# Kernel tuning notes

Hardware: AMD Instinct MI355X
Metric: run time of the kernel (lower is better)

Reference implementation:

```python
import jax, jax.numpy as jnp
import numpy as np

B, S, D, H = 2, 2048, 1024, 16
HD = D // H  # head_dim = 64
NEG = -1.0e9


def setup_inputs() -> dict:
    key = jax.random.key(0)
    ks = jax.random.split(key, 6)
    scale = 1.0 / np.sqrt(D)
    x = jax.random.normal(ks[0], (B, S, D), dtype=jnp.float32)
    # causal additive mask: 1.0 where position is masked (future), matching scores += mask * -1e9
    mask = jnp.triu(jnp.ones((S, S), dtype=jnp.float32), k=1)[None, None, :, :]
    wq = jax.random.normal(ks[1], (D, D), dtype=jnp.float32) * scale
    wk = jax.random.normal(ks[2], (D, D), dtype=jnp.float32) * scale
    wv = jax.random.normal(ks[3], (D, D), dtype=jnp.float32) * scale
    wo = jax.random.normal(ks[4], (D, D), dtype=jnp.float32) * scale
    z = jnp.zeros((D,), dtype=jnp.float32)
    return {"x": x, "mask": mask, "wq": wq, "bq": z, "wk": wk, "bk": z,
            "wv": wv, "bv": z, "wo": wo, "bo": z}


def _split_heads(t):
    # [B, S, D] -> [B, H, S, HD]
    return t.reshape(B, S, H, HD).transpose(0, 2, 1, 3)


def reference(x, mask, wq, bq, wk, bk, wv, bv, wo, bo):
    q = _split_heads(x @ wq + bq)
    k = _split_heads(x @ wk + bk)
    v = _split_heads(x @ wv + bv)
    inv_sqrt_d = 1.0 / jnp.sqrt(jnp.float32(HD))
    scores = jnp.einsum("bhqd,bhkd->bhqk", q, k) * inv_sqrt_d
    scores = scores + mask * NEG
    attn = jax.nn.softmax(scores, axis=-1)
    out = jnp.einsum("bhqk,bhkd->bhqd", attn, v)
    out = out.transpose(0, 2, 1, 3).reshape(B, S, D)  # merge heads
    return out @ wo + bo
```

## Files before the change

### kernel.cpp

```cpp
#include <hip/hip_runtime.h>
#include <hip/hip_bf16.h>


typedef __bf16 bf16x8 __attribute__((ext_vector_type(8)));
typedef float f32x4 __attribute__((ext_vector_type(4)));

#define S_LEN 2048
#define DMODEL 1024
#define NHEAD 16
#define HDIM 64
#define MROWS 4096

#define AS1 __attribute__((address_space(1)))
#define AS3 __attribute__((address_space(3)))

#define LOG2E 1.44269504f
#define QSCALE 0.18033688f

__global__ void cast_x_kernel(const float* __restrict__ X, __bf16* __restrict__ Xb) {
    int i = (blockIdx.x * blockDim.x + threadIdx.x) * 4;
    float4 f = *(const float4*)&X[i];
    Xb[i + 0] = (__bf16)f.x;
    Xb[i + 1] = (__bf16)f.y;
    Xb[i + 2] = (__bf16)f.z;
    Xb[i + 3] = (__bf16)f.w;
}

__global__ void transpose_cast_kernel(
    const float* __restrict__ W0, const float* __restrict__ W1,
    const float* __restrict__ W2, const float* __restrict__ W3,
    __bf16* __restrict__ T0, __bf16* __restrict__ T1,
    __bf16* __restrict__ T2, __bf16* __restrict__ T3) {
    const float* W = (blockIdx.z == 0) ? W0 : (blockIdx.z == 1) ? W1 : (blockIdx.z == 2) ? W2 : W3;
    __bf16* WT = (blockIdx.z == 0) ? T0 : (blockIdx.z == 1) ? T1 : (blockIdx.z == 2) ? T2 : T3;
    __shared__ float tile[32][33];
    int bx = blockIdx.x, by = blockIdx.y;
    int tx = threadIdx.x;
    for (int i = threadIdx.y; i < 32; i += 8)
        tile[i][tx] = W[(size_t)(by * 32 + i) * DMODEL + bx * 32 + tx];
    __syncthreads();
    for (int i = threadIdx.y; i < 32; i += 8)
        WT[(size_t)(bx * 32 + i) * DMODEL + by * 32 + tx] = (__bf16)tile[tx][i];
}

__global__ __launch_bounds__(256) void gemm_qkv_kernel(
    const __bf16* __restrict__ X,
    const __bf16* __restrict__ WqT, const __bf16* __restrict__ WkT, const __bf16* __restrict__ WvT,
    const float* __restrict__ bq, const float* __restrict__ bk, const float* __restrict__ bv,
    __bf16* __restrict__ Q, __bf16* __restrict__ K, __bf16* __restrict__ Vt) {
    const int which = blockIdx.z;
    const __bf16* Bt = (which == 0) ? WqT : (which == 1) ? WkT : WvT;
    const float* bias = (which == 0) ? bq : (which == 1) ? bk : bv;
    __bf16* Out = (which == 0) ? Q : (which == 1) ? K : Vt;

    __shared__ alignas(16) __bf16 As[128 * 64];
    __shared__ alignas(16) __bf16 Bs[64 * 64];

    const int tid = threadIdx.x;
    const int lane = tid & 63;
    const int wave = tid >> 6;
    const int wm = wave >> 1, wn = wave & 1;
    const int quad = lane >> 4;
    const int l16 = lane & 15;
    const int m0 = blockIdx.x * 128;
    const int n0 = blockIdx.y * 64;
    const int r8 = lane >> 3;
    const int sc8 = ((lane & 7) ^ r8) * 8;
    const int gq0 = ((0 + quad) ^ (l16 & 7)) * 8;
    const int gq1 = ((4 + quad) ^ (l16 & 7)) * 8;

    f32x4 acc[4][2] = {};

    for (int k0 = 0; k0 < DMODEL; k0 += 64) {
        __syncthreads();
#pragma unroll
        for (int p = 0; p < 4; p++) {
            const int row = wave * 32 + p * 8;
            __builtin_amdgcn_global_load_lds(
                (const AS1 void*)&X[(size_t)(m0 + row + r8) * DMODEL + k0 + sc8],
                (AS3 void*)&As[row * 64], 16, 0, 0);
        }
#pragma unroll
        for (int p = 0; p < 2; p++) {
            const int row = wave * 16 + p * 8;
            __builtin_amdgcn_global_load_lds(
                (const AS1 void*)&Bt[(size_t)(n0 + row + r8) * DMODEL + k0 + sc8],
                (AS3 void*)&Bs[row * 64], 16, 0, 0);
        }
        __syncthreads();
#pragma unroll
        for (int ks = 0; ks < 2; ks++) {
            const int g = ks ? gq1 : gq0;
            bf16x8 af[4], bfr[2];
#pragma unroll
            for (int t = 0; t < 4; t++)
                af[t] = *(bf16x8*)&As[(wm * 64 + t * 16 + l16) * 64 + g];
#pragma unroll
            for (int t = 0; t < 2; t++)
                bfr[t] = *(bf16x8*)&Bs[(wn * 32 + t * 16 + l16) * 64 + g];
#pragma unroll
            for (int mt = 0; mt < 4; mt++)
#pragma unroll
                for (int nt = 0; nt < 2; nt++)
                    acc[mt][nt] = __builtin_amdgcn_mfma_f32_16x16x32_bf16(af[mt], bfr[nt], acc[mt][nt], 0, 0, 0);
        }
    }

#pragma unroll
    for (int mt = 0; mt < 4; mt++)
#pragma unroll
        for (int nt = 0; nt < 2; nt++) {
            const int n = n0 + wn * 32 + nt * 16 + l16;
            const float bn = bias[n];
            const int h = n >> 6, hd = n & 63;
            const int mbase = m0 + wm * 64 + mt * 16 + quad * 4;
            if (which == 2) {
                __bf16 pk[4];
#pragma unroll
                for (int r = 0; r < 4; r++) pk[r] = (__bf16)(acc[mt][nt][r] + bn);
                const int m = mbase;
                const int b = m >> 11, s = m & 2047;
                *(uint2*)&Out[(((size_t)(b * NHEAD + h) * HDIM + hd) * S_LEN) + s] = *(uint2*)pk;
            } else {
                const float sc = (which == 0) ? QSCALE : 1.0f;
#pragma unroll
                for (int r = 0; r < 4; r++) {
                    const int m = mbase + r;
                    const int b = m >> 11, s = m & 2047;
                    Out[(((size_t)(b * NHEAD + h) * S_LEN + s) * HDIM) + hd] =
                        (__bf16)((acc[mt][nt][r] + bn) * sc);
                }
            }
        }
}

__global__ __launch_bounds__(256) void gemm_out_kernel(
    const __bf16* __restrict__ A, const __bf16* __restrict__ Bt,
    const float* __restrict__ bias, float* __restrict__ Y) {
    __shared__ alignas(16) __bf16 As[64 * 64];
    __shared__ alignas(16) __bf16 Bs[64 * 64];

    const int tid = threadIdx.x;
    const int lane = tid & 63;
    const int wave = tid >> 6;
    const int wm = wave >> 1, wn = wave & 1;
    const int quad = lane >> 4;
    const int l16 = lane & 15;
    const int m0 = blockIdx.x * 64;
    const int n0 = blockIdx.y * 64;
    const int r8 = lane >> 3;
    const int sc8 = ((lane & 7) ^ r8) * 8;
    const int gq0 = ((0 + quad) ^ (l16 & 7)) * 8;
    const int gq1 = ((4 + quad) ^ (l16 & 7)) * 8;

    f32x4 acc[2][2] = {};

    for (int k0 = 0; k0 < DMODEL; k0 += 64) {
        __syncthreads();
#pragma unroll
        for (int p = 0; p < 2; p++) {
            const int row = wave * 16 + p * 8;
            __builtin_amdgcn_global_load_lds(
                (const AS1 void*)&A[(size_t)(m0 + row + r8) * DMODEL + k0 + sc8],
                (AS3 void*)&As[row * 64], 16, 0, 0);
            __builtin_amdgcn_global_load_lds(
                (const AS1 void*)&Bt[(size_t)(n0 + row + r8) * DMODEL + k0 + sc8],
                (AS3 void*)&Bs[row * 64], 16, 0, 0);
        }
        __syncthreads();
#pragma unroll
        for (int ks = 0; ks < 2; ks++) {
            const int g = ks ? gq1 : gq0;
            bf16x8 af[2], bfr[2];
#pragma unroll
            for (int t = 0; t < 2; t++) {
                af[t]  = *(bf16x8*)&As[(wm * 32 + t * 16 + l16) * 64 + g];
                bfr[t] = *(bf16x8*)&Bs[(wn * 32 + t * 16 + l16) * 64 + g];
            }
#pragma unroll
            for (int mt = 0; mt < 2; mt++)
#pragma unroll
                for (int nt = 0; nt < 2; nt++)
                    acc[mt][nt] = __builtin_amdgcn_mfma_f32_16x16x32_bf16(af[mt], bfr[nt], acc[mt][nt], 0, 0, 0);
        }
    }

#pragma unroll
    for (int mt = 0; mt < 2; mt++)
#pragma unroll
        for (int nt = 0; nt < 2; nt++)
#pragma unroll
            for (int r = 0; r < 4; r++) {
                int m = m0 + wm * 32 + mt * 16 + quad * 4 + r;
                int n = n0 + wn * 32 + nt * 16 + l16;
                Y[(size_t)m * DMODEL + n] = acc[mt][nt][r] + bias[n];
            }
}

#define LDK 72

__global__ __launch_bounds__(256, 4) void attn_kernel(
    const __bf16* __restrict__ Q, const __bf16* __restrict__ K, const __bf16* __restrict__ Vt,
    __bf16* __restrict__ Aout) {
    const int id = blockIdx.x;
    const int bh = id & 31;
    const int qt = 31 - (id >> 5);
    const int b = bh >> 4, h = bh & 15;
    const int tid = threadIdx.x, lane = tid & 63, wave = tid >> 6;
    const int quad = lane >> 4, l16 = lane & 15;

    __shared__ alignas(16) __bf16 Ks[64 * 64];
    __shared__ alignas(16) __bf16 Vs[64 * 64];
    __shared__ alignas(16) __bf16 Ps[4][16 * LDK];

    const size_t base = (size_t)bh * S_LEN * HDIM;
    const int q0 = qt * 64;
    const int qrow = q0 + wave * 16 + l16;

    bf16x8 qf0 = *(const bf16x8*)&Q[base + (size_t)qrow * HDIM + quad * 8];
    bf16x8 qf1 = *(const bf16x8*)&Q[base + (size_t)qrow * HDIM + 32 + quad * 8];

    bf16x8 onef;
#pragma unroll
    for (int jj = 0; jj < 8; jj++) onef[jj] = (__bf16)1.0f;

    f32x4 oacc[4] = {};
    f32x4 lacc = {};

    const int r8 = lane >> 3;
    const int sc = (lane & 7) ^ r8;
    const int g0 = (quad ^ (l16 & 7)) * 8;
    const int g1 = g0 ^ 32;

    for (int kt = 0; kt <= qt; kt++) {
        const int k0 = kt * 64;
        __syncthreads();
#pragma unroll
        for (int p = 0; p < 2; p++) {
            const int row = wave * 16 + p * 8;
            __builtin_amdgcn_global_load_lds(
                (const AS1 void*)&K[base + (size_t)(k0 + row + r8) * HDIM + sc * 8],
                (AS3 void*)&Ks[row * 64], 16, 0, 0);
            __builtin_amdgcn_global_load_lds(
                (const AS1 void*)&Vt[base + (size_t)(row + r8) * S_LEN + k0 + sc * 8],
                (AS3 void*)&Vs[row * 64], 16, 0, 0);
        }
        __syncthreads();

        f32x4 sacc[4] = {};
#pragma unroll
        for (int nt = 0; nt < 4; nt++) {
            const int krow = (nt * 16 + l16) * 64;
            bf16x8 kf0 = *(bf16x8*)&Ks[krow + g0];
            bf16x8 kf1 = *(bf16x8*)&Ks[krow + g1];
            sacc[nt] = __builtin_amdgcn_mfma_f32_16x16x32_bf16(qf0, kf0, sacc[nt], 0, 0, 0);
            sacc[nt] = __builtin_amdgcn_mfma_f32_16x16x32_bf16(qf1, kf1, sacc[nt], 0, 0, 0);
        }

        if (kt == qt) {
#pragma unroll
            for (int nt = 0; nt < 4; nt++)
#pragma unroll
                for (int r = 0; r < 4; r++) {
                    const int kcol = k0 + nt * 16 + l16;
                    const int qg = q0 + wave * 16 + quad * 4 + r;
                    float p = (kcol > qg) ? 0.0f : __builtin_amdgcn_exp2f(sacc[nt][r]);
                    Ps[wave][(quad * 4 + r) * LDK + nt * 16 + l16] = (__bf16)p;
                }
        } else {
#pragma unroll
            for (int nt = 0; nt < 4; nt++)
#pragma unroll
                for (int r = 0; r < 4; r++)
                    Ps[wave][(quad * 4 + r) * LDK + nt * 16 + l16] =
                        (__bf16)__builtin_amdgcn_exp2f(sacc[nt][r]);
        }

        bf16x8 pf0 = *(bf16x8*)&Ps[wave][l16 * LDK + quad * 8];
        bf16x8 pf1 = *(bf16x8*)&Ps[wave][l16 * LDK + 32 + quad * 8];
#pragma unroll
        for (int nt2 = 0; nt2 < 4; nt2++) {
            const int vrow = (nt2 * 16 + l16) * 64;
            bf16x8 vf0 = *(bf16x8*)&Vs[vrow + g0];
            bf16x8 vf1 = *(bf16x8*)&Vs[vrow + g1];
            oacc[nt2] = __builtin_amdgcn_mfma_f32_16x16x32_bf16(pf0, vf0, oacc[nt2], 0, 0, 0);
            oacc[nt2] = __builtin_amdgcn_mfma_f32_16x16x32_bf16(pf1, vf1, oacc[nt2], 0, 0, 0);
        }
        lacc = __builtin_amdgcn_mfma_f32_16x16x32_bf16(pf0, onef, lacc, 0, 0, 0);
        lacc = __builtin_amdgcn_mfma_f32_16x16x32_bf16(pf1, onef, lacc, 0, 0, 0);
    }

    float rl[4];
#pragma unroll
    for (int r = 0; r < 4; r++) rl[r] = 1.0f / lacc[r];
#pragma unroll
    for (int nt2 = 0; nt2 < 4; nt2++)
#pragma unroll
        for (int r = 0; r < 4; r++) {
            int qg = q0 + wave * 16 + quad * 4 + r;
            int col = h * HDIM + nt2 * 16 + l16;
            Aout[(size_t)(b * S_LEN + qg) * DMODEL + col] = (__bf16)(oacc[nt2][r] * rl[r]);
        }
}

extern "C" void kernel_launch(void* const* d_in, const int* in_sizes, int n_in,
                              void* d_out, int out_size, void* d_ws, size_t ws_size,
                              hipStream_t stream) {
    const float* x  = (const float*)d_in[0];
    const float* wq = (const float*)d_in[2];
    const float* bq = (const float*)d_in[3];
    const float* wk = (const float*)d_in[4];
    const float* bk = (const float*)d_in[5];
    const float* wv = (const float*)d_in[6];
    const float* bv = (const float*)d_in[7];
    const float* wo = (const float*)d_in[8];
    const float* bo = (const float*)d_in[9];
    float* out = (float*)d_out;

    char* ws = (char*)d_ws;
    __bf16* xb  = (__bf16*)(ws);
    __bf16* wqT = (__bf16*)(ws + ((size_t)8  << 20));
    __bf16* wkT = (__bf16*)(ws + ((size_t)10 << 20));
    __bf16* wvT = (__bf16*)(ws + ((size_t)12 << 20));
    __bf16* woT = (__bf16*)(ws + ((size_t)14 << 20));
    __bf16* Qb  = (__bf16*)(ws + ((size_t)16 << 20));
    __bf16* Kb  = (__bf16*)(ws + ((size_t)24 << 20));
    __bf16* Vtb = (__bf16*)(ws + ((size_t)32 << 20));
    __bf16* Ab  = (__bf16*)(ws + ((size_t)40 << 20));

    cast_x_kernel<<<4096, 256, 0, stream>>>(x, xb);
    transpose_cast_kernel<<<dim3(32, 32, 4), dim3(32, 8), 0, stream>>>(
        wq, wk, wv, wo, wqT, wkT, wvT, woT);
    gemm_qkv_kernel<<<dim3(32, 16, 3), 256, 0, stream>>>(xb, wqT, wkT, wvT, bq, bk, bv, Qb, Kb, Vtb);
    attn_kernel<<<1024, 256, 0, stream>>>(Qb, Kb, Vtb, Ab);
    gemm_out_kernel<<<dim3(64, 16), 256, 0, stream>>>(Ab, woT, bo, out);
}
```

Measured before the change: 189.6 us.

## Give each attention wave two 16-row query tiles with 128-thread blocks

The attention kernel now runs 2 waves of 32 query rows each instead of 4 waves of 16 rows, launched with 128 threads per block. Each K/V fragment read from LDS is reused across two query sub-tiles, which halves LDS reads per MFMA and gives each wave more independent MFMAs to issue. The costs are more registers per wave (launch bounds changed to 128,3), fewer waves per block, and each thread issuing twice as many global-to-LDS loads for the K/V tile.

```diff
diff --git a/kernel.cpp b/kernel.cpp
--- a/kernel.cpp
+++ b/kernel.cpp
@@ -14,8 +14,8 @@
 #define AS1 __attribute__((address_space(1)))
 #define AS3 __attribute__((address_space(3)))
 
-#define LOG2E 1.44269504f
 #define QSCALE 0.18033688f
+#define LDK 72
 
 __global__ void cast_x_kernel(const float* __restrict__ X, __bf16* __restrict__ Xb) {
     int i = (blockIdx.x * blockDim.x + threadIdx.x) * 4;
@@ -197,9 +197,8 @@
             }
 }
 
-#define LDK 72
-
-__global__ __launch_bounds__(256, 4) void attn_kernel(
+
+__global__ __launch_bounds__(128, 3) void attn_kernel(
     const __bf16* __restrict__ Q, const __bf16* __restrict__ K, const __bf16* __restrict__ Vt,
     __bf16* __restrict__ Aout) {
     const int id = blockIdx.x;
@@ -211,21 +210,26 @@
 
     __shared__ alignas(16) __bf16 Ks[64 * 64];
     __shared__ alignas(16) __bf16 Vs[64 * 64];
-    __shared__ alignas(16) __bf16 Ps[4][16 * LDK];
+    __shared__ alignas(16) __bf16 Ps[2][32 * LDK];
 
     const size_t base = (size_t)bh * S_LEN * HDIM;
     const int q0 = qt * 64;
-    const int qrow = q0 + wave * 16 + l16;
-
-    bf16x8 qf0 = *(const bf16x8*)&Q[base + (size_t)qrow * HDIM + quad * 8];
-    bf16x8 qf1 = *(const bf16x8*)&Q[base + (size_t)qrow * HDIM + 32 + quad * 8];
+
+    bf16x8 qf[2][2];
+#pragma unroll
+    for (int mi = 0; mi < 2; mi++) {
+        const int qrow = q0 + wave * 32 + mi * 16 + l16;
+        qf[mi][0] = *(const bf16x8*)&Q[base + (size_t)qrow * HDIM + quad * 8];
+        qf[mi][1] = *(const bf16x8*)&Q[base + (size_t)qrow * HDIM + 32 + quad * 8];
+    }
 
     bf16x8 onef;
 #pragma unroll
     for (int jj = 0; jj < 8; jj++) onef[jj] = (__bf16)1.0f;
 
-    f32x4 oacc[4] = {};
-    f32x4 lacc = {};
+    f32x4 oacc[2][4] = {};
+    f32x4 lacc[2] = {};
+    __bf16* Psw = &Ps[wave][0];
 
     const int r8 = lane >> 3;
     const int sc = (lane & 7) ^ r8;
@@ -236,8 +240,8 @@
         const int k0 = kt * 64;
         __syncthreads();
 #pragma unroll
-        for (int p = 0; p < 2; p++) {
-            const int row = wave * 16 + p * 8;
+        for (int p = 0; p < 4; p++) {
+            const int row = wave * 32 + p * 8;
             __builtin_amdgcn_global_load_lds(
                 (const AS1 void*)&K[base + (size_t)(k0 + row + r8) * HDIM + sc * 8],
                 (AS3 void*)&Ks[row * 64], 16, 0, 0);
@@ -247,60 +251,80 @@
         }
         __syncthreads();
 
-        f32x4 sacc[4] = {};
+        f32x4 sacc[2][4] = {};
 #pragma unroll
         for (int nt = 0; nt < 4; nt++) {
             const int krow = (nt * 16 + l16) * 64;
             bf16x8 kf0 = *(bf16x8*)&Ks[krow + g0];
             bf16x8 kf1 = *(bf16x8*)&Ks[krow + g1];
-            sacc[nt] = __builtin_amdgcn_mfma_f32_16x16x32_bf16(qf0, kf0, sacc[nt], 0, 0, 0);
-            sacc[nt] = __builtin_amdgcn_mfma_f32_16x16x32_bf16(qf1, kf1, sacc[nt], 0, 0, 0);
+#pragma unroll
+            for (int mi = 0; mi < 2; mi++) {
+                sacc[mi][nt] = __builtin_amdgcn_mfma_f32_16x16x32_bf16(qf[mi][0], kf0, sacc[mi][nt], 0, 0, 0);
+                sacc[mi][nt] = __builtin_amdgcn_mfma_f32_16x16x32_bf16(qf[mi][1], kf1, sacc[mi][nt], 0, 0, 0);
+            }
         }
 
         if (kt == qt) {
 #pragma unroll
-            for (int nt = 0; nt < 4; nt++)
-#pragma unroll
-                for (int r = 0; r < 4; r++) {
-                    const int kcol = k0 + nt * 16 + l16;
-                    const int qg = q0 + wave * 16 + quad * 4 + r;
-                    float p = (kcol > qg) ? 0.0f : __builtin_amdgcn_exp2f(sacc[nt][r]);
-                    Ps[wave][(quad * 4 + r) * LDK + nt * 16 + l16] = (__bf16)p;
-                }
+            for (int mi = 0; mi < 2; mi++)
+#pragma unroll
+                for (int nt = 0; nt < 4; nt++)
+#pragma unroll
+                    for (int r = 0; r < 4; r++) {
+                        const int kcol = k0 + nt * 16 + l16;
+                        const int qg = q0 + wave * 32 + mi * 16 + quad * 4 + r;
+                        float p = (kcol > qg) ? 0.0f : __builtin_amdgcn_exp2f(sacc[mi][nt][r]);
+                        Psw[(mi * 16 + quad * 4 + r) * LDK + nt * 16 + l16] = (__bf16)p;
+                    }
         } else {
 #pragma unroll
-            for (int nt = 0; nt < 4; nt++)
-#pragma unroll
-                for (int r = 0; r < 4; r++)
-                    Ps[wave][(quad * 4 + r) * LDK + nt * 16 + l16] =
-                        (__bf16)__builtin_amdgcn_exp2f(sacc[nt][r]);
-        }
-
-        bf16x8 pf0 = *(bf16x8*)&Ps[wave][l16 * LDK + quad * 8];
-        bf16x8 pf1 = *(bf16x8*)&Ps[wave][l16 * LDK + 32 + quad * 8];
+            for (int mi = 0; mi < 2; mi++)
+#pragma unroll
+                for (int nt = 0; nt < 4; nt++)
+#pragma unroll
+                    for (int r = 0; r < 4; r++)
+                        Psw[(mi * 16 + quad * 4 + r) * LDK + nt * 16 + l16] =
+                            (__bf16)__builtin_amdgcn_exp2f(sacc[mi][nt][r]);
+        }
+
+        bf16x8 pf[2][2];
+#pragma unroll
+        for (int mi = 0; mi < 2; mi++) {
+            pf[mi][0] = *(bf16x8*)&Psw[(mi * 16 + l16) * LDK + quad * 8];
+            pf[mi][1] = *(bf16x8*)&Psw[(mi * 16 + l16) * LDK + 32 + quad * 8];
+        }
 #pragma unroll
         for (int nt2 = 0; nt2 < 4; nt2++) {
             const int vrow = (nt2 * 16 + l16) * 64;
             bf16x8 vf0 = *(bf16x8*)&Vs[vrow + g0];
             bf16x8 vf1 = *(bf16x8*)&Vs[vrow + g1];
-            oacc[nt2] = __builtin_amdgcn_mfma_f32_16x16x32_bf16(pf0, vf0, oacc[nt2], 0, 0, 0);
-            oacc[nt2] = __builtin_amdgcn_mfma_f32_16x16x32_bf16(pf1, vf1, oacc[nt2], 0, 0, 0);
-        }
-        lacc = __builtin_amdgcn_mfma_f32_16x16x32_bf16(pf0, onef, lacc, 0, 0, 0);
-        lacc = __builtin_amdgcn_mfma_f32_16x16x32_bf16(pf1, onef, lacc, 0, 0, 0);
-    }
-
-    float rl[4];
-#pragma unroll
-    for (int r = 0; r < 4; r++) rl[r] = 1.0f / lacc[r];
-#pragma unroll
-    for (int nt2 = 0; nt2 < 4; nt2++)
-#pragma unroll
-        for (int r = 0; r < 4; r++) {
-            int qg = q0 + wave * 16 + quad * 4 + r;
-            int col = h * HDIM + nt2 * 16 + l16;
-            Aout[(size_t)(b * S_LEN + qg) * DMODEL + col] = (__bf16)(oacc[nt2][r] * rl[r]);
-        }
+#pragma unroll
+            for (int mi = 0; mi < 2; mi++) {
+                oacc[mi][nt2] = __builtin_amdgcn_mfma_f32_16x16x32_bf16(pf[mi][0], vf0, oacc[mi][nt2], 0, 0, 0);
+                oacc[mi][nt2] = __builtin_amdgcn_mfma_f32_16x16x32_bf16(pf[mi][1], vf1, oacc[mi][nt2], 0, 0, 0);
+            }
+        }
+#pragma unroll
+        for (int mi = 0; mi < 2; mi++) {
+            lacc[mi] = __builtin_amdgcn_mfma_f32_16x16x32_bf16(pf[mi][0], onef, lacc[mi], 0, 0, 0);
+            lacc[mi] = __builtin_amdgcn_mfma_f32_16x16x32_bf16(pf[mi][1], onef, lacc[mi], 0, 0, 0);
+        }
+    }
+
+#pragma unroll
+    for (int mi = 0; mi < 2; mi++) {
+        float rl[4];
+#pragma unroll
+        for (int r = 0; r < 4; r++) rl[r] = 1.0f / lacc[mi][r];
+#pragma unroll
+        for (int nt2 = 0; nt2 < 4; nt2++)
+#pragma unroll
+            for (int r = 0; r < 4; r++) {
+                int qg = q0 + wave * 32 + mi * 16 + quad * 4 + r;
+                int col = h * HDIM + nt2 * 16 + l16;
+                Aout[(size_t)(b * S_LEN + qg) * DMODEL + col] = (__bf16)(oacc[mi][nt2][r] * rl[r]);
+            }
+    }
 }
 
 extern "C" void kernel_launch(void* const* d_in, const int* in_sizes, int n_in,
@@ -332,6 +356,6 @@
     transpose_cast_kernel<<<dim3(32, 32, 4), dim3(32, 8), 0, stream>>>(
         wq, wk, wv, wo, wqT, wkT, wvT, woT);
     gemm_qkv_kernel<<<dim3(32, 16, 3), 256, 0, stream>>>(xb, wqT, wkT, wvT, bq, bk, bv, Qb, Kb, Vtb);
-    attn_kernel<<<1024, 256, 0, stream>>>(Qb, Kb, Vtb, Ab);
+    attn_kernel<<<1024, 128, 0, stream>>>(Qb, Kb, Vtb, Ab);
     gemm_out_kernel<<<dim3(64, 16), 256, 0, stream>>>(Ab, woT, bo, out);
 }
```

Result: no change. 191.2 us (+0.8%).
